# Optimization experiments

Measured on AMD Instinct MI355X. Metric: run time of the kernel, lower is better.

## Reference

```python
import jax, jax.numpy as jnp
import numpy as np

B, S, HID = 2, 2048, 4096
H, KV, D = 32, 8, 128  # query heads, kv heads, head_dim
ROPE_BASE = 10000.0


def apply_rope(x, cos, sin):
    # x: (B, h, S, D); cos/sin: (S, D) broadcast over (B, h)
    x1 = x[..., ::2]
    x2 = x[..., 1::2]
    rotated = jnp.stack((-x2, x1), axis=-1).reshape(x.shape)  # interleave back
    return x * cos + rotated * sin


def setup_inputs() -> dict:
    key = jax.random.key(0)
    ks = jax.random.split(key, 5)
    hidden_states = jax.random.normal(ks[0], (B, S, HID), jnp.float32)
    # real rotary tables (interleaved convention: each freq repeated twice)
    inv_freq = 1.0 / (ROPE_BASE ** (jnp.arange(0, D, 2, dtype=jnp.float32) / D))
    freqs = jnp.arange(S, dtype=jnp.float32)[:, None] * inv_freq  # (S, D/2)
    freqs = jnp.repeat(freqs, 2, axis=-1)  # (S, D)
    cos, sin = jnp.cos(freqs), jnp.sin(freqs)
    std = 0.02
    wq = jax.random.normal(ks[1], (H * D, HID), jnp.float32) * std
    wk = jax.random.normal(ks[2], (KV * D, HID), jnp.float32) * std
    wv = jax.random.normal(ks[3], (KV * D, HID), jnp.float32) * std
    wo = jax.random.normal(ks[4], (HID, H * D), jnp.float32) * std
    return {"hidden_states": hidden_states, "cos": cos, "sin": sin,
            "wq": wq, "wk": wk, "wv": wv, "wo": wo}


def reference(hidden_states, cos, sin, wq, wk, wv, wo):
    bsz, seq, _ = hidden_states.shape
    G = H // KV  # GQA group size
    q = (hidden_states @ wq.T).reshape(bsz, seq, H, D).transpose(0, 2, 1, 3)   # (B,H,S,D)
    k = (hidden_states @ wk.T).reshape(bsz, seq, KV, D).transpose(0, 2, 1, 3)  # (B,KV,S,D)
    v = (hidden_states @ wv.T).reshape(bsz, seq, KV, D).transpose(0, 2, 1, 3)
    q = apply_rope(q, cos, sin)
    k = apply_rope(k, cos, sin)
    # GQA without materializing repeated K/V: group query heads per KV head
    qg = q.reshape(bsz, KV, G, seq, D)
    scale = 1.0 / np.float32(np.sqrt(D))
    scores = jnp.einsum('bkgsd,bktd->bkgst', qg, k) * scale  # (B,KV,G,S,S)
    causal = jnp.tril(jnp.ones((seq, seq), bool))
    scores = jnp.where(causal, scores, jnp.finfo(scores.dtype).min)
    probs = jax.nn.softmax(scores, axis=-1)
    attn = jnp.einsum('bkgst,bktd->bkgsd', probs, v)  # (B,KV,G,S,D)
    attn = attn.reshape(bsz, H, seq, D).transpose(0, 2, 1, 3).reshape(bsz, seq, H * D)
    return attn @ wo.T
```

## Files before the change

kernel.cpp:

```cpp
#include <hip/hip_runtime.h>

typedef unsigned short u16;
typedef unsigned int u32;
using bf8 = __attribute__((ext_vector_type(8))) short;
using f4  = __attribute__((ext_vector_type(4))) float;

#define DEV __device__ __forceinline__

#define QSCALE (0.08838834764831845f * 1.4426950408889634f)

DEV u16 f2b(float f) {
  u32 u = __float_as_uint(f);
  u32 r = u + 0x7fff + ((u >> 16) & 1);
  return (u16)(r >> 16);
}
DEV u32 f2b_u(u32 u) {
  return (u + 0x7fff + ((u >> 16) & 1)) >> 16;
}
DEV float b2f(u32 bits) { return __uint_as_float(bits << 16); }

#define GLOAD16(g, l)                                                          \
  __builtin_amdgcn_global_load_lds((__attribute__((address_space(1))) u32*)(g),\
                                   (__attribute__((address_space(3))) u32*)(l),\
                                   16, 0, 0)

DEV f4 mfma16(bf8 a, bf8 b, f4 c) {
  return __builtin_amdgcn_mfma_f32_16x16x32_bf16(a, b, c, 0, 0, 0);
}

__global__ __launch_bounds__(256) void convert_kernel(
    const u16* __restrict__ src, u16* __restrict__ dst,
    const u32* __restrict__ probe, int n8) {
  const int t = blockIdx.x * 256 + threadIdx.x;
  if (t >= n8) return;
  const bool isf32 = (probe[0] == 0x3F800000u);
  const uint4* s4 = (const uint4*)src;
  uint4* d4 = (uint4*)dst;
  if (!isf32) {
    d4[t] = s4[t];
    return;
  }
  uint4 a = s4[2 * t];
  uint4 b = s4[2 * t + 1];
  uint4 o;
  o.x = f2b_u(a.x) | (f2b_u(a.y) << 16);
  o.y = f2b_u(a.z) | (f2b_u(a.w) << 16);
  o.z = f2b_u(b.x) | (f2b_u(b.y) << 16);
  o.w = f2b_u(b.z) | (f2b_u(b.w) << 16);
  d4[t] = o;
}

DEV void gemm_core(const u16* __restrict__ A, const u16* __restrict__ W,
                   int lda, int ldw, int K, int mb, int nb,
                   u16* As, u16* Bs, f4 (&acc)[4][4]) {
  const int tid = threadIdx.x;
  const int lane = tid & 63;
  const int wid = tid >> 6;
  const int l16 = lane & 15;
  const int quad = lane >> 4;
  const int wm = (wid >> 1) * 64;
  const int wn = (wid & 1) * 64;

  const int c0 = wid * 2;
  const int rowA0 = c0 * 16 + (lane >> 2);
  const int colb = (lane & 3) * 16;

  const char* gA = (const char*)(A + (size_t)(mb * 128 + rowA0) * lda) + colb;
  const char* gB = (const char*)(W + (size_t)(nb * 128 + rowA0) * ldw) + colb;
  char* lA = (char*)As + c0 * 1024;
  char* lB = (char*)Bs + c0 * 1024;
  const size_t strideA = (size_t)lda * 32;
  const size_t strideB = (size_t)ldw * 32;

  for (int k0 = 0; k0 < K; k0 += 32) {
    __syncthreads();
    GLOAD16(gA + (size_t)k0 * 2, lA);
    GLOAD16(gA + (size_t)k0 * 2 + strideA, lA + 1024);
    GLOAD16(gB + (size_t)k0 * 2, lB);
    GLOAD16(gB + (size_t)k0 * 2 + strideB, lB + 1024);
    __syncthreads();

    bf8 af[4], bw[4];
#pragma unroll
    for (int t = 0; t < 4; t++) {
      af[t] = *(const bf8*)(As + (wm + t * 16 + l16) * 32 + quad * 8);
      bw[t] = *(const bf8*)(Bs + (wn + t * 16 + l16) * 32 + quad * 8);
    }
#pragma unroll
    for (int mt = 0; mt < 4; mt++)
#pragma unroll
      for (int nt = 0; nt < 4; nt++)
        acc[mt][nt] = mfma16(af[mt], bw[nt], acc[mt][nt]);
  }
}

__global__ __launch_bounds__(256) void gemm_qkv_kernel(
    const u16* __restrict__ hidden, const u16* __restrict__ wq,
    const u16* __restrict__ wk, const u16* __restrict__ wv,
    u16* __restrict__ qo, u16* __restrict__ ko, u16* __restrict__ vto) {
  __shared__ u16 As[128 * 32];
  __shared__ u16 Bs[128 * 32];
  const int mb = blockIdx.x, yb = blockIdx.y;
  const u16* W;
  u16* C;
  int nb, ldc, mode;
  if (yb < 32)      { W = wq; C = qo;  nb = yb;      ldc = 4096; mode = 0; }
  else if (yb < 40) { W = wk; C = ko;  nb = yb - 32; ldc = 1024; mode = 0; }
  else              { W = wv; C = vto; nb = yb - 40; ldc = 0;    mode = 1; }

  f4 acc[4][4];
#pragma unroll
  for (int i = 0; i < 4; i++)
#pragma unroll
    for (int j = 0; j < 4; j++) acc[i][j] = (f4){0.f, 0.f, 0.f, 0.f};

  gemm_core(hidden, W, 4096, 4096, 4096, mb, nb, As, Bs, acc);

  const int tid = threadIdx.x, lane = tid & 63, wid = tid >> 6;
  const int l16 = lane & 15, quad = lane >> 4;
  const int wm = (wid >> 1) * 64, wn = (wid & 1) * 64;

  if (mode == 0) {
#pragma unroll
    for (int mt = 0; mt < 4; mt++)
#pragma unroll
      for (int nt = 0; nt < 4; nt++) {
        const int n = nb * 128 + wn + nt * 16 + l16;
        const int m0 = mb * 128 + wm + mt * 16 + quad * 4;
#pragma unroll
        for (int r = 0; r < 4; r++)
          C[(size_t)(m0 + r) * ldc + n] = f2b(acc[mt][nt][r]);
      }
  } else {
#pragma unroll
    for (int mt = 0; mt < 4; mt++)
#pragma unroll
      for (int nt = 0; nt < 4; nt++) {
        const int n = nb * 128 + wn + nt * 16 + l16;
        const int m0 = mb * 128 + wm + mt * 16 + quad * 4;
        const int b_ = m0 >> 11, s0 = m0 & 2047;
        ushort4 pk;
        pk.x = f2b(acc[mt][nt][0]);
        pk.y = f2b(acc[mt][nt][1]);
        pk.z = f2b(acc[mt][nt][2]);
        pk.w = f2b(acc[mt][nt][3]);
        *(ushort4*)(vto + ((size_t)(b_ * 1024 + n) << 11) + s0) = pk;
      }
  }
}

__global__ __launch_bounds__(256) void gemm_o_kernel(
    const u16* __restrict__ A, const u16* __restrict__ W,
    float* __restrict__ C) {
  __shared__ u16 As[128 * 32];
  __shared__ u16 Bs[128 * 32];
  const int mb = blockIdx.x, nb = blockIdx.y;
  f4 acc[4][4];
#pragma unroll
  for (int i = 0; i < 4; i++)
#pragma unroll
    for (int j = 0; j < 4; j++) acc[i][j] = (f4){0.f, 0.f, 0.f, 0.f};

  gemm_core(A, W, 4096, 4096, 4096, mb, nb, As, Bs, acc);

  const int tid = threadIdx.x, lane = tid & 63, wid = tid >> 6;
  const int l16 = lane & 15, quad = lane >> 4;
  const int wm = (wid >> 1) * 64, wn = (wid & 1) * 64;
#pragma unroll
  for (int mt = 0; mt < 4; mt++)
#pragma unroll
    for (int nt = 0; nt < 4; nt++) {
      const int n = nb * 128 + wn + nt * 16 + l16;
      const int m0 = mb * 128 + wm + mt * 16 + quad * 4;
#pragma unroll
      for (int r = 0; r < 4; r++)
        C[(size_t)(m0 + r) * 4096 + n] = acc[mt][nt][r];
    }
}

__global__ void rope_kernel(u16* __restrict__ x, const u16* __restrict__ cs,
                            const u16* __restrict__ sn, int shift, float scale,
                            int nthreads) {
  const int t = blockIdx.x * 256 + threadIdx.x;
  if (t >= nthreads) return;
  const size_t e = (size_t)t * 8;
  const int d = (int)(e & 127);
  const int s = (int)((e >> shift) & 2047);
  uint4 xv = *(const uint4*)(x + e);
  uint4 cv = *(const uint4*)(cs + (size_t)s * 128 + d);
  uint4 sv = *(const uint4*)(sn + (size_t)s * 128 + d);
  u32 xw[4] = {xv.x, xv.y, xv.z, xv.w};
  u32 cw[4] = {cv.x, cv.y, cv.z, cv.w};
  u32 sw[4] = {sv.x, sv.y, sv.z, sv.w};
  u32 ow[4];
#pragma unroll
  for (int i = 0; i < 4; i++) {
    float x0 = b2f(xw[i] & 0xffff), x1 = b2f(xw[i] >> 16);
    float c = b2f(cw[i] & 0xffff);
    float si = b2f(sw[i] & 0xffff);
    float o0 = (x0 * c - x1 * si) * scale;
    float o1 = (x1 * c + x0 * si) * scale;
    ow[i] = (u32)f2b(o0) | ((u32)f2b(o1) << 16);
  }
  uint4 ov = {ow[0], ow[1], ow[2], ow[3]};
  *(uint4*)(x + e) = ov;
}

__global__ __launch_bounds__(256) void attn_kernel(
    const u16* __restrict__ q, const u16* __restrict__ k,
    const u16* __restrict__ vt, u16* __restrict__ attn) {
  __shared__ u16 Ks[64 * 136];
  __shared__ u16 Vt[128 * 72];
  __shared__ u16 Ps[4][16 * 72];

  const int qblk = blockIdx.x, h = blockIdx.y, b = blockIdx.z;
  const int kv = h >> 2;
  const int tid = threadIdx.x, lane = tid & 63, wid = tid >> 6;
  const int l16 = lane & 15, quad = lane >> 4;

  const u16* qp =
      q + ((size_t)(b * 2048 + qblk * 64 + wid * 16 + l16) * 32 + h) * 128;
  bf8 aq[4];
#pragma unroll
  for (int ds = 0; ds < 4; ds++)
    aq[ds] = *(const bf8*)(qp + ds * 32 + quad * 8);

  f4 accO[8];
#pragma unroll
  for (int i = 0; i < 8; i++) accO[i] = (f4){0.f, 0.f, 0.f, 0.f};
  float m = -1e30f;
  float l = 0.f;

  const u16* kp = k + ((size_t)(b * 2048) * 8 + kv) * 128;
  const u16* vp = vt + (size_t)(b * 8 + kv) * 128 * 2048;

  const int qglob = qblk * 64 + wid * 16 + l16;

  for (int kt = 0; kt <= qblk; kt++) {
    const int key0 = kt * 64;
    __syncthreads();
#pragma unroll
    for (int rep = 0; rep < 4; rep++) {
      const int e = rep * 2048 + tid * 8;
      const int row = e >> 7, col = e & 127;
      *(uint4*)(Ks + row * 136 + col) =
          *(const uint4*)(kp + (size_t)(key0 + row) * 1024 + col);
    }
#pragma unroll
    for (int rep = 0; rep < 4; rep++) {
      const int e = rep * 2048 + tid * 8;
      const int row = e >> 6, col = e & 63;
      *(uint4*)(Vt + row * 72 + col) =
          *(const uint4*)(vp + (size_t)row * 2048 + key0 + col);
    }
    __syncthreads();

    f4 sc[4];
#pragma unroll
    for (int nt = 0; nt < 4; nt++) {
      sc[nt] = (f4){0.f, 0.f, 0.f, 0.f};
      const int krow = nt * 16 + l16;
#pragma unroll
      for (int ds = 0; ds < 4; ds++) {
        bf8 bk = *(const bf8*)(Ks + krow * 136 + ds * 32 + quad * 8);
        sc[nt] = mfma16(bk, aq[ds], sc[nt]);
      }
    }

    if (kt == qblk) {
#pragma unroll
      for (int nt = 0; nt < 4; nt++)
#pragma unroll
        for (int r = 0; r < 4; r++)
          if (key0 + nt * 16 + quad * 4 + r > qglob) sc[nt][r] = -1e30f;
    }

    float mx = -1e30f;
#pragma unroll
    for (int nt = 0; nt < 4; nt++) {
      const float a = fmaxf(fmaxf(sc[nt][0], sc[nt][1]),
                            fmaxf(sc[nt][2], sc[nt][3]));
      mx = fmaxf(mx, a);
    }
    mx = fmaxf(mx, __shfl_xor(mx, 16, 64));
    mx = fmaxf(mx, __shfl_xor(mx, 32, 64));

    const bool grow = (mx - m > 8.f);
    float alpha = 1.f;
    if (grow) {
      alpha = exp2f(m - mx);
      m = mx;
      l *= alpha;
    }
    if (__ballot(grow)) {
#pragma unroll
      for (int r = 0; r < 4; r++) {
        const float ar = __shfl(alpha, (lane & 48) | (quad * 4 + r), 64);
#pragma unroll
        for (int nt = 0; nt < 8; nt++) accO[nt][r] *= ar;
      }
    }

    u16 pbits[4][4];
    float ps = 0.f;
#pragma unroll
    for (int nt = 0; nt < 4; nt++)
#pragma unroll
      for (int r = 0; r < 4; r++) {
        const float p = exp2f(sc[nt][r] - m);
        ps += p;
        pbits[nt][r] = f2b(p);
      }
    ps += __shfl_xor(ps, 16, 64);
    ps += __shfl_xor(ps, 32, 64);
    l += ps;

#pragma unroll
    for (int nt = 0; nt < 4; nt++) {
      ushort4 pk;
      pk.x = pbits[nt][0];
      pk.y = pbits[nt][1];
      pk.z = pbits[nt][2];
      pk.w = pbits[nt][3];
      *(ushort4*)(&Ps[wid][l16 * 72 + nt * 16 + quad * 4]) = pk;
    }

#pragma unroll
    for (int ks = 0; ks < 2; ks++) {
      bf8 ap = *(const bf8*)(&Ps[wid][l16 * 72 + ks * 32 + quad * 8]);
#pragma unroll
      for (int nt = 0; nt < 8; nt++) {
        bf8 bv = *(const bf8*)(Vt + (nt * 16 + l16) * 72 + ks * 32 + quad * 8);
        accO[nt] = mfma16(ap, bv, accO[nt]);
      }
    }
  }

  const float invq = 1.0f / l;
  float inv[4];
#pragma unroll
  for (int r = 0; r < 4; r++)
    inv[r] = __shfl(invq, (lane & 48) | (quad * 4 + r), 64);
#pragma unroll
  for (int nt = 0; nt < 8; nt++)
#pragma unroll
    for (int r = 0; r < 4; r++) {
      const int s = qblk * 64 + wid * 16 + quad * 4 + r;
      const int dcol = nt * 16 + l16;
      attn[((size_t)(b * 2048 + s) * 32 + h) * 128 + dcol] =
          f2b(accO[nt][r] * inv[r]);
    }
}

extern "C" void kernel_launch(void* const* d_in, const int* in_sizes, int n_in,
                              void* d_out, int out_size, void* d_ws,
                              size_t ws_size, hipStream_t stream) {
  const u16* hidden = (const u16*)d_in[0];
  const u16* cosp = (const u16*)d_in[1];
  const u16* sinp = (const u16*)d_in[2];
  const u16* wq = (const u16*)d_in[3];
  const u16* wk = (const u16*)d_in[4];
  const u16* wv = (const u16*)d_in[5];
  const u16* wo = (const u16*)d_in[6];
  const u32* probe = (const u32*)d_in[1];
  float* out = (float*)d_out;

  char* ws = (char*)d_ws;
  u16* hidden_n = (u16*)(ws);
  u16* attnb    = (u16*)(ws);
  u16* qb       = (u16*)(ws + 33554432);
  u16* kb       = (u16*)(ws + 67108864);
  u16* vtb      = (u16*)(ws + 75497472);
  u16* wq_n     = (u16*)(ws + 83886080);
  u16* wk_n     = (u16*)(ws + 117440512);
  u16* wv_n     = (u16*)(ws + 125829120);
  u16* wo_n     = (u16*)(ws + 134217728);
  u16* cos_n    = (u16*)(ws + 167772160);
  u16* sin_n    = (u16*)(ws + 168296448);

  dim3 blk(256);
  convert_kernel<<<dim3(8192), blk, 0, stream>>>(hidden, hidden_n, probe,
                                                 2097152);
  convert_kernel<<<dim3(8192), blk, 0, stream>>>(wq, wq_n, probe, 2097152);
  convert_kernel<<<dim3(2048), blk, 0, stream>>>(wk, wk_n, probe, 524288);
  convert_kernel<<<dim3(2048), blk, 0, stream>>>(wv, wv_n, probe, 524288);
  convert_kernel<<<dim3(8192), blk, 0, stream>>>(wo, wo_n, probe, 2097152);
  convert_kernel<<<dim3(128), blk, 0, stream>>>(cosp, cos_n, probe, 32768);
  convert_kernel<<<dim3(128), blk, 0, stream>>>(sinp, sin_n, probe, 32768);

  gemm_qkv_kernel<<<dim3(32, 48), blk, 0, stream>>>(hidden_n, wq_n, wk_n, wv_n,
                                                    qb, kb, vtb);
  rope_kernel<<<dim3(8192), blk, 0, stream>>>(qb, cos_n, sin_n, 12, QSCALE,
                                              2097152);
  rope_kernel<<<dim3(2048), blk, 0, stream>>>(kb, cos_n, sin_n, 10, 1.0f,
                                              524288);
  attn_kernel<<<dim3(32, 32, 2), blk, 0, stream>>>(qb, kb, vtb, attnb);
  gemm_o_kernel<<<dim3(32, 32), blk, 0, stream>>>(attnb, wo_n, out);
}
```

Measured before the change: 1.178 ms.

## Process 128 query rows per attention block with two 16-row tiles per wave

Each attention workgroup now covers 128 query rows instead of 64, and each wave handles two 16-row query tiles. Every K/V tile staged in shared memory is therefore reused by twice as many queries, and each V fragment read feeds two MFMAs. The aim is to halve the K/V global-to-LDS traffic and the block count per head. In exchange there are more registers per wave (two accumulator sets), coarser causal work balance, and some waves sit idle on the last tile. A launch-bounds occupancy hint is also added.

```diff
diff --git a/kernel.cpp b/kernel.cpp
--- a/kernel.cpp
+++ b/kernel.cpp
@@ -206,37 +206,45 @@
   *(uint4*)(x + e) = ov;
 }
 
-__global__ __launch_bounds__(256) void attn_kernel(
+__global__ __launch_bounds__(256, 2) void attn_kernel(
     const u16* __restrict__ q, const u16* __restrict__ k,
     const u16* __restrict__ vt, u16* __restrict__ attn) {
   __shared__ u16 Ks[64 * 136];
   __shared__ u16 Vt[128 * 72];
-  __shared__ u16 Ps[4][16 * 72];
+  __shared__ u16 Ps[4][32 * 72];
 
   const int qblk = blockIdx.x, h = blockIdx.y, b = blockIdx.z;
   const int kv = h >> 2;
   const int tid = threadIdx.x, lane = tid & 63, wid = tid >> 6;
   const int l16 = lane & 15, quad = lane >> 4;
 
-  const u16* qp =
-      q + ((size_t)(b * 2048 + qblk * 64 + wid * 16 + l16) * 32 + h) * 128;
-  bf8 aq[4];
-#pragma unroll
-  for (int ds = 0; ds < 4; ds++)
-    aq[ds] = *(const bf8*)(qp + ds * 32 + quad * 8);
-
-  f4 accO[8];
-#pragma unroll
-  for (int i = 0; i < 8; i++) accO[i] = (f4){0.f, 0.f, 0.f, 0.f};
-  float m = -1e30f;
-  float l = 0.f;
+  const int wq0 = qblk * 128 + wid * 32;
+
+  bf8 aq[2][4];
+#pragma unroll
+  for (int half = 0; half < 2; half++) {
+    const u16* qp =
+        q + ((size_t)(b * 2048 + wq0 + half * 16 + l16) * 32 + h) * 128;
+#pragma unroll
+    for (int ds = 0; ds < 4; ds++)
+      aq[half][ds] = *(const bf8*)(qp + ds * 32 + quad * 8);
+  }
+
+  f4 accO[2][8];
+#pragma unroll
+  for (int i = 0; i < 2; i++)
+#pragma unroll
+    for (int j = 0; j < 8; j++) accO[i][j] = (f4){0.f, 0.f, 0.f, 0.f};
+  float m_[2] = {-1e30f, -1e30f};
+  float l_[2] = {0.f, 0.f};
 
   const u16* kp = k + ((size_t)(b * 2048) * 8 + kv) * 128;
   const u16* vp = vt + (size_t)(b * 8 + kv) * 128 * 2048;
 
-  const int qglob = qblk * 64 + wid * 16 + l16;
-
-  for (int kt = 0; kt <= qblk; kt++) {
+  const int qmax = wq0 + 31;
+  const int NT = 2 * qblk + 2;
+
+  for (int kt = 0; kt < NT; kt++) {
     const int key0 = kt * 64;
     __syncthreads();
 #pragma unroll
@@ -255,101 +263,113 @@
     }
     __syncthreads();
 
-    f4 sc[4];
-#pragma unroll
-    for (int nt = 0; nt < 4; nt++) {
-      sc[nt] = (f4){0.f, 0.f, 0.f, 0.f};
-      const int krow = nt * 16 + l16;
-#pragma unroll
-      for (int ds = 0; ds < 4; ds++) {
-        bf8 bk = *(const bf8*)(Ks + krow * 136 + ds * 32 + quad * 8);
-        sc[nt] = mfma16(bk, aq[ds], sc[nt]);
-      }
+    if (key0 > qmax) continue;
+
+#pragma unroll
+    for (int half = 0; half < 2; half++) {
+      const int hq0 = wq0 + half * 16;
+      f4 sc[4];
+#pragma unroll
+      for (int nt = 0; nt < 4; nt++) {
+        sc[nt] = (f4){0.f, 0.f, 0.f, 0.f};
+        const int krow = nt * 16 + l16;
+#pragma unroll
+        for (int ds = 0; ds < 4; ds++) {
+          bf8 bk = *(const bf8*)(Ks + krow * 136 + ds * 32 + quad * 8);
+          sc[nt] = mfma16(bk, aq[half][ds], sc[nt]);
+        }
+      }
+
+      if (key0 + 63 > hq0) {
+        const int qglob = hq0 + l16;
+#pragma unroll
+        for (int nt = 0; nt < 4; nt++)
+#pragma unroll
+          for (int r = 0; r < 4; r++)
+            if (key0 + nt * 16 + quad * 4 + r > qglob) sc[nt][r] = -1e30f;
+      }
+
+      float mA = fmaxf(fmaxf(sc[0][0], sc[0][1]), fmaxf(sc[0][2], sc[0][3]));
+      float mB = fmaxf(fmaxf(sc[1][0], sc[1][1]), fmaxf(sc[1][2], sc[1][3]));
+      float mC = fmaxf(fmaxf(sc[2][0], sc[2][1]), fmaxf(sc[2][2], sc[2][3]));
+      float mD = fmaxf(fmaxf(sc[3][0], sc[3][1]), fmaxf(sc[3][2], sc[3][3]));
+      float mx = fmaxf(fmaxf(mA, mB), fmaxf(mC, mD));
+      mx = fmaxf(mx, __shfl_xor(mx, 16, 64));
+      mx = fmaxf(mx, __shfl_xor(mx, 32, 64));
+
+      const bool grow = (mx - m_[half] > 8.f);
+      float alpha = 1.f;
+      if (grow) {
+        alpha = exp2f(m_[half] - mx);
+        m_[half] = mx;
+        l_[half] *= alpha;
+      }
+      if (__ballot(grow)) {
+#pragma unroll
+        for (int r = 0; r < 4; r++) {
+          const float ar = __shfl(alpha, (lane & 48) | (quad * 4 + r), 64);
+#pragma unroll
+          for (int nt = 0; nt < 8; nt++) accO[half][nt][r] *= ar;
+        }
+      }
+
+      const float mr = m_[half];
+      float psn[4];
+#pragma unroll
+      for (int nt = 0; nt < 4; nt++) {
+        const float p0 = exp2f(sc[nt][0] - mr);
+        const float p1 = exp2f(sc[nt][1] - mr);
+        const float p2 = exp2f(sc[nt][2] - mr);
+        const float p3 = exp2f(sc[nt][3] - mr);
+        psn[nt] = (p0 + p1) + (p2 + p3);
+        ushort4 pk;
+        pk.x = f2b(p0);
+        pk.y = f2b(p1);
+        pk.z = f2b(p2);
+        pk.w = f2b(p3);
+        *(ushort4*)(&Ps[wid][(half * 16 + l16) * 72 + nt * 16 + quad * 4]) =
+            pk;
+      }
+      float ps = (psn[0] + psn[1]) + (psn[2] + psn[3]);
+      ps += __shfl_xor(ps, 16, 64);
+      ps += __shfl_xor(ps, 32, 64);
+      l_[half] += ps;
     }
 
-    if (kt == qblk) {
-#pragma unroll
-      for (int nt = 0; nt < 4; nt++)
-#pragma unroll
-        for (int r = 0; r < 4; r++)
-          if (key0 + nt * 16 + quad * 4 + r > qglob) sc[nt][r] = -1e30f;
-    }
-
-    float mx = -1e30f;
-#pragma unroll
-    for (int nt = 0; nt < 4; nt++) {
-      const float a = fmaxf(fmaxf(sc[nt][0], sc[nt][1]),
-                            fmaxf(sc[nt][2], sc[nt][3]));
-      mx = fmaxf(mx, a);
-    }
-    mx = fmaxf(mx, __shfl_xor(mx, 16, 64));
-    mx = fmaxf(mx, __shfl_xor(mx, 32, 64));
-
-    const bool grow = (mx - m > 8.f);
-    float alpha = 1.f;
-    if (grow) {
-      alpha = exp2f(m - mx);
-      m = mx;
-      l *= alpha;
-    }
-    if (__ballot(grow)) {
-#pragma unroll
-      for (int r = 0; r < 4; r++) {
-        const float ar = __shfl(alpha, (lane & 48) | (quad * 4 + r), 64);
-#pragma unroll
-        for (int nt = 0; nt < 8; nt++) accO[nt][r] *= ar;
-      }
-    }
-
-    u16 pbits[4][4];
-    float ps = 0.f;
-#pragma unroll
-    for (int nt = 0; nt < 4; nt++)
-#pragma unroll
-      for (int r = 0; r < 4; r++) {
-        const float p = exp2f(sc[nt][r] - m);
-        ps += p;
-        pbits[nt][r] = f2b(p);
-      }
-    ps += __shfl_xor(ps, 16, 64);
-    ps += __shfl_xor(ps, 32, 64);
-    l += ps;
-
-#pragma unroll
-    for (int nt = 0; nt < 4; nt++) {
-      ushort4 pk;
-      pk.x = pbits[nt][0];
-      pk.y = pbits[nt][1];
-      pk.z = pbits[nt][2];
-      pk.w = pbits[nt][3];
-      *(ushort4*)(&Ps[wid][l16 * 72 + nt * 16 + quad * 4]) = pk;
-    }
-
-#pragma unroll
-    for (int ks = 0; ks < 2; ks++) {
-      bf8 ap = *(const bf8*)(&Ps[wid][l16 * 72 + ks * 32 + quad * 8]);
+    bf8 ap[2][2];
+#pragma unroll
+    for (int half = 0; half < 2; half++)
+#pragma unroll
+      for (int ks = 0; ks < 2; ks++)
+        ap[half][ks] = *(const bf8*)(&Ps[wid][(half * 16 + l16) * 72 +
+                                             ks * 32 + quad * 8]);
+#pragma unroll
+    for (int ks = 0; ks < 2; ks++)
 #pragma unroll
       for (int nt = 0; nt < 8; nt++) {
         bf8 bv = *(const bf8*)(Vt + (nt * 16 + l16) * 72 + ks * 32 + quad * 8);
-        accO[nt] = mfma16(ap, bv, accO[nt]);
-      }
-    }
-  }
-
-  const float invq = 1.0f / l;
-  float inv[4];
-#pragma unroll
-  for (int r = 0; r < 4; r++)
-    inv[r] = __shfl(invq, (lane & 48) | (quad * 4 + r), 64);
-#pragma unroll
-  for (int nt = 0; nt < 8; nt++)
-#pragma unroll
-    for (int r = 0; r < 4; r++) {
-      const int s = qblk * 64 + wid * 16 + quad * 4 + r;
-      const int dcol = nt * 16 + l16;
-      attn[((size_t)(b * 2048 + s) * 32 + h) * 128 + dcol] =
-          f2b(accO[nt][r] * inv[r]);
-    }
+        accO[0][nt] = mfma16(ap[0][ks], bv, accO[0][nt]);
+        accO[1][nt] = mfma16(ap[1][ks], bv, accO[1][nt]);
+      }
+  }
+
+#pragma unroll
+  for (int half = 0; half < 2; half++) {
+    const float invq = 1.0f / l_[half];
+    float inv[4];
+#pragma unroll
+    for (int r = 0; r < 4; r++)
+      inv[r] = __shfl(invq, (lane & 48) | (quad * 4 + r), 64);
+#pragma unroll
+    for (int nt = 0; nt < 8; nt++)
+#pragma unroll
+      for (int r = 0; r < 4; r++) {
+        const int s = wq0 + half * 16 + quad * 4 + r;
+        const int dcol = nt * 16 + l16;
+        attn[((size_t)(b * 2048 + s) * 32 + h) * 128 + dcol] =
+            f2b(accO[half][nt][r] * inv[r]);
+      }
+  }
 }
 
 extern "C" void kernel_launch(void* const* d_in, const int* in_sizes, int n_in,
@@ -394,6 +414,6 @@
                                               2097152);
   rope_kernel<<<dim3(2048), blk, 0, stream>>>(kb, cos_n, sin_n, 10, 1.0f,
                                               524288);
-  attn_kernel<<<dim3(32, 32, 2), blk, 0, stream>>>(qb, kb, vtb, attnb);
+  attn_kernel<<<dim3(16, 32, 2), blk, 0, stream>>>(qb, kb, vtb, attnb);
   gemm_o_kernel<<<dim3(32, 32), blk, 0, stream>>>(attnb, wo_n, out);
 }
```

Result: faster. 1.006 ms (-14.6%).
